# Optimization experiments

Hardware: AMD Instinct MI355X
Metric: run time of the kernel (lower is better)

Reference implementation:

```python
import jax, jax.numpy as jnp
import numpy as np

ROUTINGS = 3


def squash(v):
    # squash along last axis: v/|v| * |v|^2/(1+|v|^2)
    norm = jnp.linalg.norm(v, axis=-1, keepdims=True)
    ns = norm * norm
    return v / norm * (ns / (1.0 + ns))


def setup_inputs() -> dict:
    key = jax.random.key(0)
    k1, k2 = jax.random.split(key)
    B, N, I, D, Din = 256, 10, 1152, 16, 8
    inputs = jax.random.normal(k1, (B, I, Din), dtype=jnp.float32)
    # glorot-uniform-ish init for W [N, I, D, Din]
    limit = np.sqrt(6.0 / (D + Din)).astype(np.float32)
    W = jax.random.uniform(k2, (N, I, D, Din), dtype=jnp.float32,
                           minval=-limit, maxval=limit)
    return {"inputs": inputs, "W": W}


def reference(inputs, W):
    # inputs: [B, I, Din], W: [N, I, D, Din]
    # u_hat[b,n,i,d] = sum_k W[n,i,d,k] * inputs[b,i,k]  (replaces tf.map_fn)
    u_hat = jnp.einsum('nidk,bik->bnid', W, inputs)  # [B, N, I, D]
    b = jnp.zeros(u_hat.shape[:3], dtype=u_hat.dtype)  # [B, N, I]
    outputs = None
    for r in range(ROUTINGS):
        c = jax.nn.softmax(b, axis=1)  # softmax over output capsules N
        outputs = squash(jnp.einsum('bni,bnid->bnd', c, u_hat))  # [B, N, D]
        if r < ROUTINGS - 1:
            # agreement: a[b,n,i] = <outputs[b,n,:], u_hat[b,n,i,:]>
            b = b + jnp.einsum('bnd,bnid->bni', outputs, u_hat)
    return outputs
```

## Files before the change

### kernel.cpp

```cpp
#include <hip/hip_runtime.h>
#include <stdint.h>


#define BN 256
#define NN 10
#define II 1152
#define DD 16
#define KK 8
#define NT 18
#define NCH 3
#define CHI 384

typedef unsigned short ushort_t;
typedef unsigned int uint_t;

__device__ __forceinline__ float bflo(uint_t u) {
    union { uint_t i; float f; } v; v.i = u << 16; return v.f;
}
__device__ __forceinline__ float bfhi(uint_t u) {
    union { uint_t i; float f; } v; v.i = u & 0xffff0000u; return v.f;
}
__device__ __forceinline__ uint_t f2bf(float f) {
    union { float f; uint_t i; } v; v.f = f;
    uint_t x = v.i;
    return (x + 0x7fffu + ((x >> 16) & 1u)) >> 16;
}

__global__ __launch_bounds__(256) void caps_uhat_s0(const float* __restrict__ xg,
                                                    const float* __restrict__ wg,
                                                    ushort_t* __restrict__ u,
                                                    float* __restrict__ part0,
                                                    int b0, int c4)
{
    __shared__ float red[16][NN][16];
    const int tid = threadIdx.x;
    const int lane = tid & 63, wv = tid >> 6;
    const int dq = lane & 3, il = lane >> 2;
    const int it = blockIdx.x / c4;
    const int bl = (blockIdx.x % c4) * 4;
    const int i = it * 64 + wv * 16 + il;

    float xv[4][8];
#pragma unroll
    for (int bb = 0; bb < 4; ++bb) {
        const float4* xp = (const float4*)(xg + ((size_t)(b0 + bl + bb) * II + i) * KK);
        float4 x0 = xp[0], x1 = xp[1];
        xv[bb][0] = x0.x; xv[bb][1] = x0.y; xv[bb][2] = x0.z; xv[bb][3] = x0.w;
        xv[bb][4] = x1.x; xv[bb][5] = x1.y; xv[bb][6] = x1.z; xv[bb][7] = x1.w;
    }

    for (int n = 0; n < NN; ++n) {
        const float4* wp = (const float4*)(wg + (size_t)(n * II + i) * (DD * KK)) + dq * 8;
        float4 w[8];
#pragma unroll
        for (int j = 0; j < 8; ++j) w[j] = wp[j];

        float s[4][4];
#pragma unroll
        for (int dj = 0; dj < 4; ++dj) {
            float4 wa = w[2 * dj], wb = w[2 * dj + 1];
#pragma unroll
            for (int bb = 0; bb < 4; ++bb) {
                s[bb][dj] = wa.x * xv[bb][0] + wa.y * xv[bb][1]
                          + wa.z * xv[bb][2] + wa.w * xv[bb][3]
                          + wb.x * xv[bb][4] + wb.y * xv[bb][5]
                          + wb.z * xv[bb][6] + wb.w * xv[bb][7];
            }
        }
#pragma unroll
        for (int bb = 0; bb < 4; ++bb) {
            uint2 q;
            q.x = f2bf(s[bb][0]) | (f2bf(s[bb][1]) << 16);
            q.y = f2bf(s[bb][2]) | (f2bf(s[bb][3]) << 16);
            *(uint2*)(u + (((size_t)(bl + bb) * NN + n) * II + i) * DD + dq * 4) = q;
        }
#pragma unroll
        for (int m = 4; m <= 32; m <<= 1)
#pragma unroll
            for (int bb = 0; bb < 4; ++bb)
#pragma unroll
                for (int dj = 0; dj < 4; ++dj)
                    s[bb][dj] += __shfl_xor(s[bb][dj], m, 64);
        if (il == 0) {
#pragma unroll
            for (int bb = 0; bb < 4; ++bb)
#pragma unroll
                for (int dj = 0; dj < 4; ++dj)
                    red[wv * 4 + dq][n][bb * 4 + dj] = s[bb][dj];
        }
    }
    __syncthreads();
#pragma unroll
    for (int idx = tid; idx < 640; idx += 256) {
        int bb = idx / 160, r = idx - bb * 160;
        int n = r >> 4, d = r & 15, q2 = d >> 2, dj = d & 3;
        float v = red[0 + q2][n][bb * 4 + dj] + red[4 + q2][n][bb * 4 + dj]
                + red[8 + q2][n][bb * 4 + dj] + red[12 + q2][n][bb * 4 + dj];
        part0[((size_t)(b0 + bl + bb) * NT + it) * 160 + r] = 0.1f * v;
    }
}

__device__ __forceinline__ void block_reduce_part(float sp[NN][4], int tid,
                                                  float* red,
                                                  float* __restrict__ partp)
{
#pragma unroll
    for (int m = 4; m <= 32; m <<= 1)
#pragma unroll
        for (int n = 0; n < NN; ++n)
#pragma unroll
            for (int j = 0; j < 4; ++j)
                sp[n][j] += __shfl_xor(sp[n][j], m, 64);

    const int lane = tid & 63, wv = tid >> 6, ld = tid & 3;
    if (lane < 4) {
#pragma unroll
        for (int n = 0; n < NN; ++n)
#pragma unroll
            for (int j = 0; j < 4; ++j)
                red[(wv * NN + n) * 16 + ld * 4 + j] = sp[n][j];
    }
    __syncthreads();
    if (tid < 160) {
        int n = tid >> 4, dd = tid & 15;
        float v = 0.f;
#pragma unroll
        for (int w = 0; w < 4; ++w) v += red[(w * NN + n) * 16 + dd];
        partp[tid] = v;
    }
}

__global__ __launch_bounds__(256) void caps_sweep(const ushort_t* __restrict__ u,
                                                  const float* __restrict__ p0,
                                                  const float* __restrict__ p1,
                                                  float* __restrict__ pout, int b0)
{
    __shared__ float red[4 * 160];
    __shared__ float o_s[160];
    const int tid = threadIdx.x, g = tid >> 2, ld = tid & 3;
    const int cb = blockIdx.x / NCH, ch = blockIdx.x % NCH;
    const int b = b0 + cb;
    const ushort_t* ub = u + (size_t)cb * (NN * II * DD);

    if (tid < 160) {
        float v = 0.f;
#pragma unroll
        for (int t = 0; t < NT; ++t)
            v += p0[((size_t)b * NT + t) * 160 + tid];
        float sq = v * v;
#pragma unroll
        for (int m = 1; m <= 8; m <<= 1) sq += __shfl_xor(sq, m, 64);
        float o = v * (sqrtf(sq) / (1.0f + sq));
        if (p1) {
            float v1 = 0.f;
#pragma unroll
            for (int c2 = 0; c2 < NCH; ++c2)
                v1 += p1[((size_t)b * NCH + c2) * 160 + tid];
            float sq1 = v1 * v1;
#pragma unroll
            for (int m = 1; m <= 8; m <<= 1) sq1 += __shfl_xor(sq1, m, 64);
            o += v1 * (sqrtf(sq1) / (1.0f + sq1));
        }
        o_s[tid] = o;
    }
    __syncthreads();

    float sp[NN][4];
#pragma unroll
    for (int n = 0; n < NN; ++n)
#pragma unroll
        for (int j = 0; j < 4; ++j) sp[n][j] = 0.f;

    for (int step = 0; step < CHI / 64; ++step) {
        int i = ch * CHI + step * 64 + g;
        uint2 r[NN];
#pragma unroll
        for (int n = 0; n < NN; ++n)
            r[n] = *(const uint2*)(ub + ((size_t)(n * II + i)) * DD + ld * 4);

        float p[NN];
#pragma unroll
        for (int n = 0; n < NN; ++n) {
            float4 o4 = *(const float4*)&o_s[(n << 4) + (ld << 2)];
            p[n] = bflo(r[n].x) * o4.x + bfhi(r[n].x) * o4.y
                 + bflo(r[n].y) * o4.z + bfhi(r[n].y) * o4.w;
        }
        float a[NN];
#pragma unroll
        for (int n = 0; n < NN; ++n) {
            float t2 = p[n] + __shfl_xor(p[n], 1, 64);
            a[n] = t2 + __shfl_xor(t2, 2, 64);
        }
        float m = a[0];
#pragma unroll
        for (int n = 1; n < NN; ++n) m = fmaxf(m, a[n]);
        float c[NN], ssum = 0.f;
#pragma unroll
        for (int n = 0; n < NN; ++n) { c[n] = __expf(a[n] - m); ssum += c[n]; }
        float inv = 1.0f / ssum;
#pragma unroll
        for (int n = 0; n < NN; ++n) {
            float w = c[n] * inv;
            sp[n][0] += w * bflo(r[n].x); sp[n][1] += w * bfhi(r[n].x);
            sp[n][2] += w * bflo(r[n].y); sp[n][3] += w * bfhi(r[n].y);
        }
    }
    block_reduce_part(sp, tid, red, pout + ((size_t)b * NCH + ch) * 160);
}

__global__ __launch_bounds__(192) void caps_out(const float* __restrict__ p2,
                                                float* __restrict__ out, int b0)
{
    const int b = b0 + blockIdx.x;
    const int t = threadIdx.x;
    if (t < 160) {
        float v = 0.f;
#pragma unroll
        for (int ch = 0; ch < NCH; ++ch)
            v += p2[((size_t)b * NCH + ch) * 160 + t];
        float sq = v * v;
#pragma unroll
        for (int m = 1; m <= 8; m <<= 1) sq += __shfl_xor(sq, m, 64);
        out[(size_t)b * 160 + t] = v * (sqrtf(sq) / (1.0f + sq));
    }
}

extern "C" void kernel_launch(void* const* d_in, const int* in_sizes, int n_in,
                              void* d_out, int out_size, void* d_ws, size_t ws_size,
                              hipStream_t stream)
{
    const float* xg = (const float*)d_in[0];
    const float* wg = (const float*)d_in[1];
    if (n_in >= 2 && in_sizes[0] == NN * II * DD * KK) {
        const float* t = xg; xg = wg; wg = t;
    }
    float* outp = (float*)d_out;

    const size_t perB  = (size_t)NN * II * DD * 2;
    const size_t p0B   = (size_t)BN * NT * 160 * 4;
    const size_t p12B  = (size_t)BN * NCH * 160 * 4;
    size_t extra = p0B + 2 * p12B;
    size_t avail = (ws_size > extra) ? ws_size - extra : 0;
    int C = 256;
    if (avail < (size_t)256 * perB) {
        C = (int)(avail / perB);
        C &= ~15;
        if (C < 16) C = 16;
    }
    ushort_t* uws = (ushort_t*)d_ws;
    float* part0 = (float*)((char*)d_ws + (size_t)C * perB);
    float* part1 = part0 + (size_t)BN * NT * 160;
    float* part2 = part1 + (size_t)BN * NCH * 160;

    for (int b0 = 0; b0 < BN; b0 += C) {
        int c = (BN - b0 < C) ? (BN - b0) : C;
        int c4 = c / 4;
        caps_uhat_s0<<<NT * c4, 256, 0, stream>>>(xg, wg, uws, part0, b0, c4);
        caps_sweep  <<<c * NCH, 256, 0, stream>>>(uws, part0, nullptr, part1, b0);
        caps_sweep  <<<c * NCH, 256, 0, stream>>>(uws, part0, part1,  part2, b0);
        caps_out    <<<c,       192, 0, stream>>>(part2, outp, b0);
    }
}
```

Measured before the change: 155.3 us.

## Prefetch u_hat rows in routing loop, double chunk count, remap blocks, use hw bf16 pack

The routing kernel now loads the next step's u_hat rows into registers while the current step computes, a software double-buffer meant to hide global load latency. The chunk count goes from 3 to 6 with half the rows per chunk, giving more blocks for parallelism. The u_hat producer remaps block indices in strides of 8 (likely aimed at the MI355X's XCD layout) and replaces manual bf16 rounding with the HIP intrinsic pack. The prefetch adds register pressure, and more chunks add partial-sum reduction work.

```diff
diff --git a/kernel.cpp b/kernel.cpp
--- a/kernel.cpp
+++ b/kernel.cpp
@@ -1,4 +1,5 @@
 #include <hip/hip_runtime.h>
+#include <hip/hip_bf16.h>
 #include <stdint.h>
 
 
@@ -8,8 +9,8 @@
 #define DD 16
 #define KK 8
 #define NT 18
-#define NCH 3
-#define CHI 384
+#define NCH 6
+#define CHI 192
 
 typedef unsigned short ushort_t;
 typedef unsigned int uint_t;
@@ -20,10 +21,9 @@
 __device__ __forceinline__ float bfhi(uint_t u) {
     union { uint_t i; float f; } v; v.i = u & 0xffff0000u; return v.f;
 }
-__device__ __forceinline__ uint_t f2bf(float f) {
-    union { float f; uint_t i; } v; v.f = f;
-    uint_t x = v.i;
-    return (x + 0x7fffu + ((x >> 16) & 1u)) >> 16;
+__device__ __forceinline__ uint_t pkbf(float lo, float hi) {
+    __hip_bfloat162 h = __float22bfloat162_rn(make_float2(lo, hi));
+    uint_t u; __builtin_memcpy(&u, &h, sizeof(u)); return u;
 }
 
 __global__ __launch_bounds__(256) void caps_uhat_s0(const float* __restrict__ xg,
@@ -36,8 +36,10 @@
     const int tid = threadIdx.x;
     const int lane = tid & 63, wv = tid >> 6;
     const int dq = lane & 3, il = lane >> 2;
-    const int it = blockIdx.x / c4;
-    const int bl = (blockIdx.x % c4) * 4;
+    const int nb8 = gridDim.x >> 3;
+    const int L   = (blockIdx.x & 7) * nb8 + (blockIdx.x >> 3);
+    const int it  = L / c4;
+    const int bl  = (L - it * c4) * 4;
     const int i = it * 64 + wv * 16 + il;
 
     float xv[4][8];
@@ -70,8 +72,8 @@
 #pragma unroll
         for (int bb = 0; bb < 4; ++bb) {
             uint2 q;
-            q.x = f2bf(s[bb][0]) | (f2bf(s[bb][1]) << 16);
-            q.y = f2bf(s[bb][2]) | (f2bf(s[bb][3]) << 16);
+            q.x = pkbf(s[bb][0], s[bb][1]);
+            q.y = pkbf(s[bb][2], s[bb][3]);
             *(uint2*)(u + (((size_t)(bl + bb) * NN + n) * II + i) * DD + dq * 4) = q;
         }
 #pragma unroll
@@ -171,12 +173,21 @@
 #pragma unroll
         for (int j = 0; j < 4; ++j) sp[n][j] = 0.f;
 
+    const int i0 = ch * CHI + g;
+    uint2 r[NN];
+#pragma unroll
+    for (int n = 0; n < NN; ++n)
+        r[n] = *(const uint2*)(ub + ((size_t)(n * II + i0)) * DD + ld * 4);
+
+#pragma unroll
     for (int step = 0; step < CHI / 64; ++step) {
-        int i = ch * CHI + step * 64 + g;
-        uint2 r[NN];
-#pragma unroll
-        for (int n = 0; n < NN; ++n)
-            r[n] = *(const uint2*)(ub + ((size_t)(n * II + i)) * DD + ld * 4);
+        uint2 rn[NN];
+        if (step + 1 < CHI / 64) {
+            const int i2 = i0 + (step + 1) * 64;
+#pragma unroll
+            for (int n = 0; n < NN; ++n)
+                rn[n] = *(const uint2*)(ub + ((size_t)(n * II + i2)) * DD + ld * 4);
+        }
 
         float p[NN];
 #pragma unroll
@@ -203,6 +214,10 @@
             float w = c[n] * inv;
             sp[n][0] += w * bflo(r[n].x); sp[n][1] += w * bfhi(r[n].x);
             sp[n][2] += w * bflo(r[n].y); sp[n][3] += w * bfhi(r[n].y);
+        }
+        if (step + 1 < CHI / 64) {
+#pragma unroll
+            for (int n = 0; n < NN; ++n) r[n] = rn[n];
         }
     }
     block_reduce_part(sp, tid, red, pout + ((size_t)b * NCH + ch) * 160);
```

Result: slower. 168.6 us (+8.6%).
